# Kernel tuning notes

Measured on AMD Instinct MI355X. Metric: run time of the kernel, lower is better.

The kernel has to match this reference:

```python
import jax, jax.numpy as jnp
import numpy as np


def setup_inputs() -> dict:
    key = jax.random.key(0)
    k1, k2 = jax.random.split(key)
    N, C, T, K = 8192, 3, 2048, 10
    Xt = jax.random.normal(k1, (N, C, T), dtype=jnp.float32)
    y_true = jax.random.randint(k2, (N,), 0, K, dtype=jnp.int64)
    return {"Xt": Xt, "y_true": y_true, "num_classes": K}


def reference(Xt, y_true, num_classes):
    # Within-Class Sum of Squares: for each class k,
    #   loss_k = mean((Xk - mean(Xk, axis=0))**2)  (mean over all elements)
    # total = mean over classes. Assumes all num_classes labels are present
    # (matches torch.unique iteration under this data distribution).
    N = Xt.shape[0]
    D = Xt.shape[1] * Xt.shape[2]  # elements per sample
    sums = jax.ops.segment_sum(Xt, y_true, num_segments=num_classes)        # [K, C, T]
    counts = jax.ops.segment_sum(jnp.ones((N,), Xt.dtype), y_true,
                                 num_segments=num_classes)                  # [K]
    means = sums / counts[:, None, None]                                    # [K, C, T]
    sq = jnp.square(Xt - means[y_true])                                     # [N, C, T]
    sq_per_sample = sq.reshape(N, -1).sum(axis=1)                           # [N]
    sq_sums = jax.ops.segment_sum(sq_per_sample, y_true,
                                  num_segments=num_classes)                 # [K]
    per_class_mse = sq_sums / (counts * D)                                  # [K]
    return per_class_mse.mean()
```

## Files before the change

kernel.cpp:

```cpp
#include <hip/hip_runtime.h>

#define N_SAMP 8192
#define D_DIM 6144
#define K_CLS 10
#define RWIN 256
#define NWIN2 (N_SAMP / RWIN)
#define CG 24
#define TPB 64
#define NBLK (CG * NWIN2)

typedef float f4 __attribute__((ext_vector_type(4)));

__device__ __forceinline__ void atom_add_dev(float* p, float v) {
    __hip_atomic_fetch_add(p, v, __ATOMIC_RELAXED, __HIP_MEMORY_SCOPE_AGENT);
}
__device__ __forceinline__ float load_dev(const float* p) {
    return __hip_atomic_load(p, __ATOMIC_RELAXED, __HIP_MEMORY_SCOPE_AGENT);
}
__device__ __forceinline__ float wave_sum(float x) {
#pragma unroll
    for (int o = 32; o > 0; o >>= 1) x += __shfl_down(x, o, 64);
    return x;
}

__global__ __launch_bounds__(1024) void build_sort(const int* __restrict__ y,
                                                   int* __restrict__ counts,
                                                   int* __restrict__ sorted,
                                                   float* __restrict__ S1,
                                                   float* __restrict__ s2sum,
                                                   unsigned* __restrict__ ctr,
                                                   int4* __restrict__ win_meta) {
    __shared__ int M[K_CLS * 1024];
    __shared__ int wsum[16];
    __shared__ int cls_start[K_CLS + 1];
    const int tid = threadIdx.x;
    const int lane = tid & 63;
    const int wid = tid >> 6;

    {
        f4 z = {0.f, 0.f, 0.f, 0.f};
        f4* p = (f4*)S1;
#pragma unroll
        for (int i = 0; i < (K_CLS * D_DIM) / (4 * 1024); ++i)
            p[i * 1024 + tid] = z;
        if (tid < K_CLS) s2sum[tid] = 0.f;
        if (tid == K_CLS) *ctr = 0u;
    }

    const int base = tid * 8;
    const int4 ya = ((const int4*)y)[tid * 2];
    const int4 yb = ((const int4*)y)[tid * 2 + 1];
    int yy[8] = {ya.x, ya.y, ya.z, ya.w, yb.x, yb.y, yb.z, yb.w};
    int h[K_CLS];
#pragma unroll
    for (int k = 0; k < K_CLS; ++k) h[k] = 0;
#pragma unroll
    for (int i = 0; i < 8; ++i)
#pragma unroll
        for (int k = 0; k < K_CLS; ++k) h[k] += (yy[i] == k) ? 1 : 0;
#pragma unroll
    for (int k = 0; k < K_CLS; ++k) M[k * 1024 + tid] = h[k];
    __syncthreads();

    int loc[K_CLS];
    int run = 0;
#pragma unroll
    for (int j = 0; j < K_CLS; ++j) { loc[j] = run; run += M[tid * K_CLS + j]; }
    int v = run;
#pragma unroll
    for (int d = 1; d < 64; d <<= 1) {
        int n = __shfl_up(v, d, 64);
        if (lane >= d) v += n;
    }
    if (lane == 63) wsum[wid] = v;
    __syncthreads();
    int wbase = 0;
#pragma unroll
    for (int w = 0; w < 16; ++w) wbase += (w < wid) ? wsum[w] : 0;
    const int tbase = wbase + (v - run);
    __syncthreads();
#pragma unroll
    for (int j = 0; j < K_CLS; ++j) M[tid * K_CLS + j] = tbase + loc[j];
    __syncthreads();

    if (tid < K_CLS) {
        const int s = M[tid * 1024];
        const int e = (tid == K_CLS - 1) ? N_SAMP : M[(tid + 1) * 1024];
        counts[tid] = e - s;
        cls_start[tid] = s;
        if (tid == 0) cls_start[K_CLS] = N_SAMP;
    }
    __syncthreads();

    if (tid < NWIN2) {
        const int lo = tid * RWIN, hi = lo + RWIN;
        int kA = 0;
#pragma unroll
        for (int k = 0; k < K_CLS; ++k)
            if (cls_start[k] <= lo) kA = k;
        const int bnd = cls_start[kA + 1];
        const int bpos = (bnd < hi) ? (bnd - lo) : RWIN;
        const int kB = (bpos < RWIN) ? (kA + 1) : kA;
        win_meta[tid] = make_int4(bpos, kA, kB, 0);
    }

    int off[K_CLS];
#pragma unroll
    for (int k = 0; k < K_CLS; ++k) off[k] = M[k * 1024 + tid];
#pragma unroll
    for (int i = 0; i < 8; ++i)
#pragma unroll
        for (int k = 0; k < K_CLS; ++k)
            if (yy[i] == k) sorted[off[k]++] = (k << 16) | (base + i);
}

__global__ __launch_bounds__(TPB) void wcss_accum(const float* __restrict__ X,
                                                  const int* __restrict__ sorted,
                                                  const int4* __restrict__ win_meta,
                                                  const int* __restrict__ counts,
                                                  float* __restrict__ S1,
                                                  float* __restrict__ s2sum,
                                                  unsigned* __restrict__ ctr,
                                                  float* __restrict__ out) {
    __shared__ int off_lds[RWIN];
    const int tid = threadIdx.x;
    const int wy = blockIdx.y;
    const int col0 = blockIdx.x * (TPB * 4) + tid * 4;

    {
        const int4 pp = ((const int4*)(sorted + wy * RWIN))[tid];
        off_lds[tid * 4 + 0] = (pp.x & 0xffff) * (D_DIM * 4);
        off_lds[tid * 4 + 1] = (pp.y & 0xffff) * (D_DIM * 4);
        off_lds[tid * 4 + 2] = (pp.z & 0xffff) * (D_DIM * 4);
        off_lds[tid * 4 + 3] = (pp.w & 0xffff) * (D_DIM * 4);
    }
    __syncthreads();

    const int4 meta = win_meta[wy];
    const int bpos = __builtin_amdgcn_readfirstlane(meta.x);
    const int kA   = __builtin_amdgcn_readfirstlane(meta.y);
    const int kB   = __builtin_amdgcn_readfirstlane(meta.z);

    const char* xb = (const char*)X + (size_t)col0 * 4;

#define LOADR(r) (*(const f4*)(xb + (size_t)(unsigned) \
        __builtin_amdgcn_readfirstlane(off_lds[(r)])))
#define CONSUME(V) { a1 += (V); \
        s2c += (V).x*(V).x + (V).y*(V).y + (V).z*(V).z + (V).w*(V).w; }

    f4 a1; float s2c; int r;
#define SEG(sBeg, sEnd, KC)                                                  \
    {                                                                        \
        a1 = (f4){0.f, 0.f, 0.f, 0.f}; s2c = 0.f;                            \
        r = (sBeg);                                                          \
        for (; r + 8 <= (sEnd); r += 8) {        \
            f4 v0 = LOADR(r+0), v1 = LOADR(r+1), v2 = LOADR(r+2),            \
               v3 = LOADR(r+3), v4 = LOADR(r+4), v5 = LOADR(r+5),            \
               v6 = LOADR(r+6), v7 = LOADR(r+7);                             \
            asm volatile("" :: "v"(v0), "v"(v1), "v"(v2), "v"(v3),           \
                               "v"(v4), "v"(v5), "v"(v6), "v"(v7));          \
            CONSUME(v0) CONSUME(v1) CONSUME(v2) CONSUME(v3)                  \
            CONSUME(v4) CONSUME(v5) CONSUME(v6) CONSUME(v7)                  \
        }                                                                    \
        for (; r < (sEnd); ++r) { f4 vv = LOADR(r); CONSUME(vv) }            \
        float* p1 = S1 + (KC) * D_DIM + col0;                                \
        atom_add_dev(p1 + 0, a1.x); atom_add_dev(p1 + 1, a1.y);              \
        atom_add_dev(p1 + 2, a1.z); atom_add_dev(p1 + 3, a1.w);              \
        float rs_ = wave_sum(s2c);                                           \
        if (tid == 0) atom_add_dev(&s2sum[(KC)], rs_);                       \
    }

    SEG(0, bpos, kA)
    if (bpos < RWIN) { SEG(bpos, RWIN, kB) }
#undef SEG
#undef CONSUME
#undef LOADR

    asm volatile("s_waitcnt vmcnt(0)" ::: "memory");
    unsigned t = 0;
    if (tid == 0)
        t = __hip_atomic_fetch_add(ctr, 1u, __ATOMIC_RELAXED,
                                   __HIP_MEMORY_SCOPE_AGENT);
    t = __shfl((int)t, 0, 64);
    if (t != (unsigned)(NBLK - 1)) return;

    float part = 0.f;
#pragma unroll
    for (int k = 0; k < K_CLS; ++k) {
        const float c = (float)counts[k];
        const float inv2 = 1.0f / (c * c * (float)D_DIM * (float)K_CLS);
        const float* Sk = S1 + k * D_DIM;
        for (int j = 0; j < D_DIM / TPB; ++j) {
            float vv = load_dev(&Sk[j * TPB + tid]);
            part -= vv * vv * inv2;
        }
        if (tid == 0)
            part += load_dev(&s2sum[k]) / (c * (float)D_DIM * (float)K_CLS);
    }
    float rr = wave_sum(part);
    if (tid == 0) *out = rr;
}

extern "C" void kernel_launch(void* const* d_in, const int* in_sizes, int n_in,
                              void* d_out, int out_size, void* d_ws, size_t ws_size,
                              hipStream_t stream) {
    const float* X = (const float*)d_in[0];
    const int* y = (const int*)d_in[1];

    float* S1 = (float*)d_ws;
    float* s2sum = S1 + K_CLS * D_DIM;
    int* counts = (int*)(s2sum + K_CLS);
    unsigned* ctr = (unsigned*)(counts + K_CLS);
    char* p = (char*)(ctr + 1);
    p += (16 - ((uintptr_t)p & 15)) & 15;
    int4* win_meta = (int4*)p;
    int* sorted = (int*)(win_meta + NWIN2);
    float* out = (float*)d_out;

    build_sort<<<dim3(1), dim3(1024), 0, stream>>>(y, counts, sorted,
                                                   S1, s2sum, ctr, win_meta);
    wcss_accum<<<dim3(CG, NWIN2), dim3(TPB), 0, stream>>>(X, sorted, win_meta,
                                                          counts, S1, s2sum,
                                                          ctr, out);
}
```

Measured before the change: 324.3 us.

## Split row window across four waves and move finalization to separate kernel

Each block now has four wavefronts instead of one. Each wave handles 64 of the 256 sorted rows for the same 256 columns, so the 24x32 grid keeps more loads in flight per CU. Per-wave partial sums are reduced in LDS before a single set of atomics, so atomic traffic stays the same. The last-block counter and its serial single-wave finalization are replaced by a separate 60-block finish kernel, which adds a launch and depends on atomicAdd into the output, which build_sort now zeroes.

Result: faster. 298.9 us (-7.8%).

```diff
diff --git a/kernel.cpp b/kernel.cpp
--- a/kernel.cpp
+++ b/kernel.cpp
@@ -5,17 +5,16 @@
 #define K_CLS 10
 #define RWIN 256
 #define NWIN2 (N_SAMP / RWIN)
-#define CG 24
-#define TPB 64
-#define NBLK (CG * NWIN2)
+#define CGW 24
+#define TPB 256
+#define RPW 64
+#define FIN_COLS 1024
+#define FIN_G (D_DIM / FIN_COLS)
 
 typedef float f4 __attribute__((ext_vector_type(4)));
 
 __device__ __forceinline__ void atom_add_dev(float* p, float v) {
     __hip_atomic_fetch_add(p, v, __ATOMIC_RELAXED, __HIP_MEMORY_SCOPE_AGENT);
-}
-__device__ __forceinline__ float load_dev(const float* p) {
-    return __hip_atomic_load(p, __ATOMIC_RELAXED, __HIP_MEMORY_SCOPE_AGENT);
 }
 __device__ __forceinline__ float wave_sum(float x) {
 #pragma unroll
@@ -28,8 +27,8 @@
                                                    int* __restrict__ sorted,
                                                    float* __restrict__ S1,
                                                    float* __restrict__ s2sum,
-                                                   unsigned* __restrict__ ctr,
-                                                   int4* __restrict__ win_meta) {
+                                                   int4* __restrict__ win_meta,
+                                                   float* __restrict__ out) {
     __shared__ int M[K_CLS * 1024];
     __shared__ int wsum[16];
     __shared__ int cls_start[K_CLS + 1];
@@ -44,7 +43,7 @@
         for (int i = 0; i < (K_CLS * D_DIM) / (4 * 1024); ++i)
             p[i * 1024 + tid] = z;
         if (tid < K_CLS) s2sum[tid] = 0.f;
-        if (tid == K_CLS) *ctr = 0u;
+        if (tid == K_CLS) *out = 0.f;
     }
 
     const int base = tid * 8;
@@ -114,91 +113,112 @@
             if (yy[i] == k) sorted[off[k]++] = (k << 16) | (base + i);
 }
 
-__global__ __launch_bounds__(TPB) void wcss_accum(const float* __restrict__ X,
-                                                  const int* __restrict__ sorted,
-                                                  const int4* __restrict__ win_meta,
-                                                  const int* __restrict__ counts,
-                                                  float* __restrict__ S1,
-                                                  float* __restrict__ s2sum,
-                                                  unsigned* __restrict__ ctr,
-                                                  float* __restrict__ out) {
+__global__ __launch_bounds__(TPB, 4) void wcss_accum(const float* __restrict__ X,
+                                                     const int* __restrict__ sorted,
+                                                     const int4* __restrict__ win_meta,
+                                                     float* __restrict__ S1,
+                                                     float* __restrict__ s2sum) {
     __shared__ int off_lds[RWIN];
+    __shared__ f4 redA[4][64];
+    __shared__ f4 redB[4][64];
+    __shared__ float s2red[8];
     const int tid = threadIdx.x;
+    const int lane = tid & 63;
+    const int wid = tid >> 6;
     const int wy = blockIdx.y;
-    const int col0 = blockIdx.x * (TPB * 4) + tid * 4;
-
-    {
-        const int4 pp = ((const int4*)(sorted + wy * RWIN))[tid];
-        off_lds[tid * 4 + 0] = (pp.x & 0xffff) * (D_DIM * 4);
-        off_lds[tid * 4 + 1] = (pp.y & 0xffff) * (D_DIM * 4);
-        off_lds[tid * 4 + 2] = (pp.z & 0xffff) * (D_DIM * 4);
-        off_lds[tid * 4 + 3] = (pp.w & 0xffff) * (D_DIM * 4);
-    }
+    const int col0 = blockIdx.x * 256 + lane * 4;
+
+    off_lds[tid] = (sorted[wy * RWIN + tid] & 0xffff) * (D_DIM * 4);
     __syncthreads();
 
     const int4 meta = win_meta[wy];
     const int bpos = __builtin_amdgcn_readfirstlane(meta.x);
     const int kA   = __builtin_amdgcn_readfirstlane(meta.y);
     const int kB   = __builtin_amdgcn_readfirstlane(meta.z);
+    const int wbeg = wid * RPW;
+    const int wend = wbeg + RPW;
 
     const char* xb = (const char*)X + (size_t)col0 * 4;
 
 #define LOADR(r) (*(const f4*)(xb + (size_t)(unsigned) \
         __builtin_amdgcn_readfirstlane(off_lds[(r)])))
-#define CONSUME(V) { a1 += (V); \
-        s2c += (V).x*(V).x + (V).y*(V).y + (V).z*(V).z + (V).w*(V).w; }
-
-    f4 a1; float s2c; int r;
-#define SEG(sBeg, sEnd, KC)                                                  \
+#define CONSUME(ACC, S2, V) { ACC += (V); \
+        S2 += (V).x*(V).x + (V).y*(V).y + (V).z*(V).z + (V).w*(V).w; }
+#define SEGLOOP(sBeg, sEnd, ACC, S2)                                         \
     {                                                                        \
-        a1 = (f4){0.f, 0.f, 0.f, 0.f}; s2c = 0.f;                            \
-        r = (sBeg);                                                          \
-        for (; r + 8 <= (sEnd); r += 8) {        \
+        int r = (sBeg);                                                      \
+        for (; r + 8 <= (sEnd); r += 8) {             \
             f4 v0 = LOADR(r+0), v1 = LOADR(r+1), v2 = LOADR(r+2),            \
                v3 = LOADR(r+3), v4 = LOADR(r+4), v5 = LOADR(r+5),            \
                v6 = LOADR(r+6), v7 = LOADR(r+7);                             \
             asm volatile("" :: "v"(v0), "v"(v1), "v"(v2), "v"(v3),           \
                                "v"(v4), "v"(v5), "v"(v6), "v"(v7));          \
-            CONSUME(v0) CONSUME(v1) CONSUME(v2) CONSUME(v3)                  \
-            CONSUME(v4) CONSUME(v5) CONSUME(v6) CONSUME(v7)                  \
+            CONSUME(ACC, S2, v0) CONSUME(ACC, S2, v1)                        \
+            CONSUME(ACC, S2, v2) CONSUME(ACC, S2, v3)                        \
+            CONSUME(ACC, S2, v4) CONSUME(ACC, S2, v5)                        \
+            CONSUME(ACC, S2, v6) CONSUME(ACC, S2, v7)                        \
         }                                                                    \
-        for (; r < (sEnd); ++r) { f4 vv = LOADR(r); CONSUME(vv) }            \
-        float* p1 = S1 + (KC) * D_DIM + col0;                                \
-        atom_add_dev(p1 + 0, a1.x); atom_add_dev(p1 + 1, a1.y);              \
-        atom_add_dev(p1 + 2, a1.z); atom_add_dev(p1 + 3, a1.w);              \
-        float rs_ = wave_sum(s2c);                                           \
-        if (tid == 0) atom_add_dev(&s2sum[(KC)], rs_);                       \
-    }
-
-    SEG(0, bpos, kA)
-    if (bpos < RWIN) { SEG(bpos, RWIN, kB) }
-#undef SEG
+        for (; r < (sEnd); ++r) { f4 vv = LOADR(r); CONSUME(ACC, S2, vv) }   \
+    }
+
+    f4 aA = {0.f, 0.f, 0.f, 0.f}, aB = {0.f, 0.f, 0.f, 0.f};
+    float s2A = 0.f, s2B = 0.f;
+
+    { const int aEnd = (bpos < wend) ? bpos : wend;
+      if (aEnd > wbeg) SEGLOOP(wbeg, aEnd, aA, s2A) }
+    { const int bBeg = (bpos > wbeg) ? bpos : wbeg;
+      if (bBeg < wend) SEGLOOP(bBeg, wend, aB, s2B) }
+#undef SEGLOOP
 #undef CONSUME
 #undef LOADR
 
-    asm volatile("s_waitcnt vmcnt(0)" ::: "memory");
-    unsigned t = 0;
-    if (tid == 0)
-        t = __hip_atomic_fetch_add(ctr, 1u, __ATOMIC_RELAXED,
-                                   __HIP_MEMORY_SCOPE_AGENT);
-    t = __shfl((int)t, 0, 64);
-    if (t != (unsigned)(NBLK - 1)) return;
-
-    float part = 0.f;
-#pragma unroll
-    for (int k = 0; k < K_CLS; ++k) {
-        const float c = (float)counts[k];
-        const float inv2 = 1.0f / (c * c * (float)D_DIM * (float)K_CLS);
-        const float* Sk = S1 + k * D_DIM;
-        for (int j = 0; j < D_DIM / TPB; ++j) {
-            float vv = load_dev(&Sk[j * TPB + tid]);
-            part -= vv * vv * inv2;
-        }
-        if (tid == 0)
-            part += load_dev(&s2sum[k]) / (c * (float)D_DIM * (float)K_CLS);
-    }
-    float rr = wave_sum(part);
-    if (tid == 0) *out = rr;
+    redA[wid][lane] = aA;
+    redB[wid][lane] = aB;
+    const float rA = wave_sum(s2A);
+    const float rB = wave_sum(s2B);
+    if (lane == 0) { s2red[wid] = rA; s2red[4 + wid] = rB; }
+    __syncthreads();
+
+    if (wid == 0) {
+        const f4 s = redA[0][lane] + redA[1][lane] + redA[2][lane] + redA[3][lane];
+        float* p1 = S1 + kA * D_DIM + col0;
+        atom_add_dev(p1 + 0, s.x); atom_add_dev(p1 + 1, s.y);
+        atom_add_dev(p1 + 2, s.z); atom_add_dev(p1 + 3, s.w);
+        if (lane == 0)
+            atom_add_dev(&s2sum[kA], s2red[0] + s2red[1] + s2red[2] + s2red[3]);
+    } else if (wid == 1 && bpos < RWIN) {
+        const f4 s = redB[0][lane] + redB[1][lane] + redB[2][lane] + redB[3][lane];
+        float* p1 = S1 + kB * D_DIM + col0;
+        atom_add_dev(p1 + 0, s.x); atom_add_dev(p1 + 1, s.y);
+        atom_add_dev(p1 + 2, s.z); atom_add_dev(p1 + 3, s.w);
+        if (lane == 0)
+            atom_add_dev(&s2sum[kB], s2red[4] + s2red[5] + s2red[6] + s2red[7]);
+    }
+}
+
+__global__ __launch_bounds__(256) void wcss_finish(const float* __restrict__ S1,
+                                                   const float* __restrict__ s2sum,
+                                                   const int* __restrict__ counts,
+                                                   float* __restrict__ out) {
+    __shared__ float sbuf[256];
+    const int tid = threadIdx.x;
+    const int k = blockIdx.x / FIN_G;
+    const int g = blockIdx.x % FIN_G;
+    const float cnt = (float)counts[k];
+    const float inv = 1.0f / (cnt * cnt * (float)D_DIM * (float)K_CLS);
+
+    const f4 v = *(const f4*)(S1 + k * D_DIM + g * FIN_COLS + tid * 4);
+    float t = -(v.x * v.x + v.y * v.y + v.z * v.z + v.w * v.w) * inv;
+    if (g == 0 && tid == 0)
+        t += s2sum[k] / (cnt * (float)D_DIM * (float)K_CLS);
+
+    sbuf[tid] = t;
+    __syncthreads();
+    for (int off = 128; off > 0; off >>= 1) {
+        if (tid < off) sbuf[tid] += sbuf[tid + off];
+        __syncthreads();
+    }
+    if (tid == 0) atomicAdd(out, sbuf[0]);
 }
 
 extern "C" void kernel_launch(void* const* d_in, const int* in_sizes, int n_in,
@@ -210,16 +230,16 @@
     float* S1 = (float*)d_ws;
     float* s2sum = S1 + K_CLS * D_DIM;
     int* counts = (int*)(s2sum + K_CLS);
-    unsigned* ctr = (unsigned*)(counts + K_CLS);
-    char* p = (char*)(ctr + 1);
+    char* p = (char*)(counts + K_CLS);
     p += (16 - ((uintptr_t)p & 15)) & 15;
     int4* win_meta = (int4*)p;
     int* sorted = (int*)(win_meta + NWIN2);
     float* out = (float*)d_out;
 
     build_sort<<<dim3(1), dim3(1024), 0, stream>>>(y, counts, sorted,
-                                                   S1, s2sum, ctr, win_meta);
-    wcss_accum<<<dim3(CG, NWIN2), dim3(TPB), 0, stream>>>(X, sorted, win_meta,
-                                                          counts, S1, s2sum,
-                                                          ctr, out);
-}
+                                                   S1, s2sum, win_meta, out);
+    wcss_accum<<<dim3(CGW, NWIN2), dim3(TPB), 0, stream>>>(X, sorted, win_meta,
+                                                           S1, s2sum);
+    wcss_finish<<<dim3(K_CLS * FIN_G), dim3(256), 0, stream>>>(S1, s2sum,
+                                                               counts, out);
+}
```
